# Performance work log

Measured on AMD Instinct MI355X. Metric: run time of the kernel, lower is better.

## Reference

```python
import jax, jax.numpy as jnp
import numpy as np

N_NODES = 50000
N_EDGES = 600000
N_FEAT = 128
HIDDEN = 128
OUT_CH = 128
N_GRAPHS = 64
BN_EPS = 1e-5


def gcn_conv(x, src, dst, ew, W, b):
    """PyG GCNConv: add self-loops, symmetric deg^{-1/2} normalization with edge weights."""
    n = x.shape[0]
    h = x @ W  # [N, out]
    loop = jnp.arange(n)
    src2 = jnp.concatenate([src, loop])
    dst2 = jnp.concatenate([dst, loop])
    w2 = jnp.concatenate([ew, jnp.ones((n,), x.dtype)])
    deg = jax.ops.segment_sum(w2, dst2, num_segments=n)
    dinv = jnp.where(deg > 0, jax.lax.rsqrt(deg), 0.0)
    norm = dinv[src2] * w2 * dinv[dst2]  # [E+N]
    out = jax.ops.segment_sum(h[src2] * norm[:, None], dst2, num_segments=n)
    return out + b


def setup_inputs() -> dict:
    key = jax.random.key(0)
    ks = jax.random.split(key, 12)
    x = jax.random.normal(ks[0], (N_NODES, N_FEAT), jnp.float32)
    edge_index = jax.random.randint(ks[1], (2, N_EDGES), 0, N_NODES, dtype=jnp.int64)
    batch = jnp.sort(jax.random.randint(ks[2], (N_NODES,), 0, N_GRAPHS, dtype=jnp.int64))
    edge_attr = jax.random.uniform(ks[3], (N_EDGES,), jnp.float32)
    s1 = 1.0 / np.sqrt(N_FEAT)
    s2 = 1.0 / np.sqrt(HIDDEN)
    s3 = 1.0 / np.sqrt(OUT_CH)
    s4 = 1.0 / np.sqrt(OUT_CH // 2)
    return {
        "x": x, "edge_index": edge_index, "batch": batch, "edge_attr": edge_attr,
        "W1": jax.random.uniform(ks[4], (N_FEAT, HIDDEN), jnp.float32, -s1, s1),
        "b1": jnp.zeros((HIDDEN,), jnp.float32),
        "W2": jax.random.uniform(ks[5], (HIDDEN, OUT_CH), jnp.float32, -s2, s2),
        "b2": jnp.zeros((OUT_CH,), jnp.float32),
        "fc1_W": jax.random.uniform(ks[6], (OUT_CH, OUT_CH // 2), jnp.float32, -s3, s3),
        "fc1_b": jax.random.uniform(ks[7], (OUT_CH // 2,), jnp.float32, -s3, s3),
        "bn_gamma": jnp.ones((OUT_CH // 2,), jnp.float32),
        "bn_beta": jnp.zeros((OUT_CH // 2,), jnp.float32),
        "fc3_W": jax.random.uniform(ks[8], (OUT_CH // 2, 1), jnp.float32, -s4, s4),
        "fc3_b": jax.random.uniform(ks[9], (1,), jnp.float32, -s4, s4),
    }


def reference(x, edge_index, batch, edge_attr, W1, b1, W2, b2,
              fc1_W, fc1_b, bn_gamma, bn_beta, fc3_W, fc3_b):
    src, dst = edge_index[0], edge_index[1]
    h = jax.nn.relu(gcn_conv(x, src, dst, edge_attr, W1, b1))
    # dropout skipped (deterministic eval: mode=False)
    h = jax.nn.relu(gcn_conv(h, src, dst, edge_attr, W2, b2))
    # global_mean_pool over batch segment ids
    sums = jax.ops.segment_sum(h, batch, num_segments=N_GRAPHS)  # [G, out]
    cnt = jax.ops.segment_sum(jnp.ones_like(batch, jnp.float32), batch, num_segments=N_GRAPHS)
    g = sums / jnp.maximum(cnt, 1.0)[:, None]
    z = jax.nn.relu(g @ fc1_W + fc1_b)
    # BatchNorm1d with batch statistics (training-mode math, biased var)
    mean = jnp.mean(z, axis=0)
    var = jnp.mean((z - mean) ** 2, axis=0)
    z = bn_gamma * (z - mean) * jax.lax.rsqrt(var + BN_EPS) + bn_beta
    return z @ fc3_W + fc3_b  # [G, 1]
```

## Files before the change

kernel.cpp:

```cpp
#include <hip/hip_runtime.h>

#define NNODES 50000
#define NEDGES 600000
#define NGRAPHS 64
#define BN_EPS 1e-5f
#define NB1 ((NNODES + 255) / 256)
#define PPG 16
#define GEMM_BLOCKS ((NNODES + 127) / 128)
#define COUNT_BLOCKS 512


__device__ __forceinline__ void gemm_tile(const float* __restrict__ A,
        const float* __restrict__ W, float* __restrict__ C, int block) {
    __shared__ float a_lds[32][132];
    __shared__ float w_lds[32][192];
    const int tid = threadIdx.x;
    const int row0 = block * 128;
    const int tx = tid & 15;
    const int ty = tid >> 4;
    float acc[8][8];
#pragma unroll
    for (int i = 0; i < 8; ++i)
#pragma unroll
        for (int j = 0; j < 8; ++j) acc[i][j] = 0.f;

    for (int kc = 0; kc < 128; kc += 32) {
#pragma unroll
        for (int p = 0; p < 4; ++p) {
            int idx = p * 256 + tid;
            int r = idx >> 3;
            int k4 = (idx & 7) << 2;
            int grow = row0 + r;
            float4 v = make_float4(0.f, 0.f, 0.f, 0.f);
            if (grow < NNODES) v = *(const float4*)(A + (size_t)grow * 128 + kc + k4);
            a_lds[k4 + 0][r] = v.x; a_lds[k4 + 1][r] = v.y;
            a_lds[k4 + 2][r] = v.z; a_lds[k4 + 3][r] = v.w;
        }
#pragma unroll
        for (int p = 0; p < 4; ++p) {
            int idx = p * 256 + tid;
            int kk = idx >> 5;
            int c4 = idx & 31;
            float4 v = *(const float4*)(W + (size_t)(kc + kk) * 128 + c4 * 4);
            int sw = 12 * (c4 >> 1) + ((c4 & 1) << 2);
            *(float4*)&w_lds[kk][sw] = v;
        }
        __syncthreads();
#pragma unroll
        for (int k = 0; k < 32; ++k) {
            float a[8], b[8];
            *(float4*)&a[0] = *(const float4*)&a_lds[k][ty * 8];
            *(float4*)&a[4] = *(const float4*)&a_lds[k][ty * 8 + 4];
            *(float4*)&b[0] = *(const float4*)&w_lds[k][tx * 12];
            *(float4*)&b[4] = *(const float4*)&w_lds[k][tx * 12 + 4];
#pragma unroll
            for (int i = 0; i < 8; ++i)
#pragma unroll
                for (int j = 0; j < 8; ++j)
                    acc[i][j] = fmaf(a[i], b[j], acc[i][j]);
        }
        __syncthreads();
    }
#pragma unroll
    for (int i = 0; i < 8; ++i) {
        int grow = row0 + ty * 8 + i;
        if (grow < NNODES) {
            float4 v0 = make_float4(acc[i][0], acc[i][1], acc[i][2], acc[i][3]);
            float4 v1 = make_float4(acc[i][4], acc[i][5], acc[i][6], acc[i][7]);
            *(float4*)(C + (size_t)grow * 128 + tx * 8) = v0;
            *(float4*)(C + (size_t)grow * 128 + tx * 8 + 4) = v1;
        }
    }
}

__global__ __launch_bounds__(256) void k_gemm1_count(const float* __restrict__ A,
        const float* __restrict__ W, float* __restrict__ C,
        const int* __restrict__ dst, int* __restrict__ cnt, int* __restrict__ rank) {
    if (blockIdx.x >= GEMM_BLOCKS) {
        int b = blockIdx.x - GEMM_BLOCKS;
        for (int e = b * 256 + threadIdx.x; e < NEDGES; e += COUNT_BLOCKS * 256) {
            int d = dst[e];
            rank[e] = atomicAdd(&cnt[d], 1);
        }
        return;
    }
    gemm_tile(A, W, C, blockIdx.x);
}

__global__ __launch_bounds__(256) void k_gemm(const float* __restrict__ A,
        const float* __restrict__ W, float* __restrict__ C) {
    gemm_tile(A, W, C, blockIdx.x);
}


__global__ __launch_bounds__(256) void k_scan1(const int* __restrict__ cnt,
        int* __restrict__ excl, int* __restrict__ bsum) {
    __shared__ int sh[256];
    int b = blockIdx.x, t = threadIdx.x;
    int idx = b * 256 + t;
    int v = (idx < NNODES) ? cnt[idx] : 0;
    sh[t] = v;
    __syncthreads();
#pragma unroll
    for (int off = 1; off < 256; off <<= 1) {
        int x = (t >= off) ? sh[t - off] : 0;
        __syncthreads();
        sh[t] += x;
        __syncthreads();
    }
    if (idx < NNODES) excl[idx] = sh[t] - v;
    if (t == 255) bsum[b] = sh[255];
}

__global__ __launch_bounds__(256) void k_scan2(int* __restrict__ bsum) {
    __shared__ int sh[256];
    int t = threadIdx.x;
    int v = (t < NB1) ? bsum[t] : 0;
    sh[t] = v;
    __syncthreads();
#pragma unroll
    for (int off = 1; off < 256; off <<= 1) {
        int x = (t >= off) ? sh[t - off] : 0;
        __syncthreads();
        sh[t] += x;
        __syncthreads();
    }
    if (t < NB1) bsum[t] = sh[t] - v;
}

__global__ __launch_bounds__(256) void k_scan3(const int* __restrict__ excl,
        const int* __restrict__ bsum, int* __restrict__ row_start) {
    int b = blockIdx.x, t = threadIdx.x;
    int idx = b * 256 + t;
    if (idx < NNODES) row_start[idx] = excl[idx] + bsum[b];
    if (idx == 0) row_start[NNODES] = NEDGES;
}


__global__ __launch_bounds__(256) void k_place(const int* __restrict__ src,
        const int* __restrict__ dst, const float* __restrict__ ew,
        const int* __restrict__ rank, const int* __restrict__ row_start,
        int2* __restrict__ csr_pk) {
    int e = blockIdx.x * 256 + threadIdx.x;
    if (e < NEDGES) {
        int d = dst[e];
        int slot = row_start[d] + rank[e];
        csr_pk[slot] = make_int2(src[e], __float_as_int(ew[e]));
    }
}

__global__ __launch_bounds__(256) void k_deg(const int* __restrict__ row_start,
        const int2* __restrict__ csr_pk, float* __restrict__ dinv) {
    int i = blockIdx.x * 256 + threadIdx.x;
    if (i >= NNODES) return;
    int e0 = row_start[i], e1 = row_start[i + 1];
    float deg = 1.f;
    for (int e = e0; e < e1; ++e) deg += __int_as_float(csr_pk[e].y);
    dinv[i] = rsqrtf(deg);
}

__global__ __launch_bounds__(256) void k_wfill(const int* __restrict__ row_start,
        int2* __restrict__ csr_pk, const float* __restrict__ dinv) {
    int i = blockIdx.x * 256 + threadIdx.x;
    if (i >= NNODES) return;
    int e0 = row_start[i], e1 = row_start[i + 1];
    float di = dinv[i];
    for (int e = e0; e < e1; ++e) {
        int2 pk = csr_pk[e];
        float w = dinv[pk.x] * __int_as_float(pk.y) * di;
        csr_pk[e].y = __float_as_int(w);
    }
}


__global__ __launch_bounds__(256) void k_aggregate(const float* __restrict__ h,
        const float* __restrict__ dinv, const int* __restrict__ row_start,
        const int2* __restrict__ csr_pk, const float* __restrict__ bias,
        float* __restrict__ out) {
    int gtid = blockIdx.x * 256 + threadIdx.x;
    int i = gtid >> 5;
    int lane = (gtid & 31) << 2;
    if (i >= NNODES) return;
    float di = dinv[i];
    float sw = di * di;
    float4 hv = *(const float4*)(h + (size_t)i * 128 + lane);
    float ax = sw * hv.x, ay = sw * hv.y, az = sw * hv.z, aw = sw * hv.w;
    int e = row_start[i];
    int e1 = row_start[i + 1];
    for (; e + 3 < e1; e += 4) {
        int2 p0 = csr_pk[e], p1 = csr_pk[e + 1], p2 = csr_pk[e + 2], p3 = csr_pk[e + 3];
        float4 v0 = *(const float4*)(h + (size_t)p0.x * 128 + lane);
        float4 v1 = *(const float4*)(h + (size_t)p1.x * 128 + lane);
        float4 v2 = *(const float4*)(h + (size_t)p2.x * 128 + lane);
        float4 v3 = *(const float4*)(h + (size_t)p3.x * 128 + lane);
        float w0 = __int_as_float(p0.y), w1 = __int_as_float(p1.y);
        float w2 = __int_as_float(p2.y), w3 = __int_as_float(p3.y);
        ax = fmaf(w0, v0.x, ax); ay = fmaf(w0, v0.y, ay);
        az = fmaf(w0, v0.z, az); aw = fmaf(w0, v0.w, aw);
        ax = fmaf(w1, v1.x, ax); ay = fmaf(w1, v1.y, ay);
        az = fmaf(w1, v1.z, az); aw = fmaf(w1, v1.w, aw);
        ax = fmaf(w2, v2.x, ax); ay = fmaf(w2, v2.y, ay);
        az = fmaf(w2, v2.z, az); aw = fmaf(w2, v2.w, aw);
        ax = fmaf(w3, v3.x, ax); ay = fmaf(w3, v3.y, ay);
        az = fmaf(w3, v3.z, az); aw = fmaf(w3, v3.w, aw);
    }
    for (; e < e1; ++e) {
        int2 p0 = csr_pk[e];
        float w0 = __int_as_float(p0.y);
        float4 v0 = *(const float4*)(h + (size_t)p0.x * 128 + lane);
        ax = fmaf(w0, v0.x, ax); ay = fmaf(w0, v0.y, ay);
        az = fmaf(w0, v0.z, az); aw = fmaf(w0, v0.w, aw);
    }
    float4 b = *(const float4*)(bias + lane);
    float4 o;
    o.x = fmaxf(ax + b.x, 0.f);
    o.y = fmaxf(ay + b.y, 0.f);
    o.z = fmaxf(az + b.z, 0.f);
    o.w = fmaxf(aw + b.w, 0.f);
    *(float4*)(out + (size_t)i * 128 + lane) = o;
}


__global__ __launch_bounds__(256) void k_pool1(const float* __restrict__ h2,
        const int* __restrict__ batch, float* __restrict__ part) {
    __shared__ float sh[256];
    int g = blockIdx.x / PPG;
    int p = blockIdx.x % PPG;
    int t = threadIdx.x;
    int lo = 0, hi = NNODES;
    while (lo < hi) { int mid = (lo + hi) >> 1; if (batch[mid] < g) lo = mid + 1; else hi = mid; }
    int b0 = lo;
    lo = 0; hi = NNODES;
    int g1 = g + 1;
    while (lo < hi) { int mid = (lo + hi) >> 1; if (batch[mid] < g1) lo = mid + 1; else hi = mid; }
    int b1 = lo;

    int c = t & 127, q = t >> 7;
    float acc = 0.f;
    for (int r = b0 + p * 2 + q; r < b1; r += PPG * 2) acc += h2[(size_t)r * 128 + c];
    sh[t] = acc;
    __syncthreads();
    if (t < 128) part[((size_t)g * PPG + p) * 128 + t] = sh[t] + sh[t + 128];
}

__global__ __launch_bounds__(128) void k_pool2(const float* __restrict__ part,
        const int* __restrict__ batch, float* __restrict__ gmean) {
    int g = blockIdx.x;
    int t = threadIdx.x;
    int lo = 0, hi = NNODES;
    while (lo < hi) { int mid = (lo + hi) >> 1; if (batch[mid] < g) lo = mid + 1; else hi = mid; }
    int b0 = lo;
    lo = 0; hi = NNODES;
    int g1 = g + 1;
    while (lo < hi) { int mid = (lo + hi) >> 1; if (batch[mid] < g1) lo = mid + 1; else hi = mid; }
    int b1 = lo;
    float s = 0.f;
#pragma unroll
    for (int p = 0; p < PPG; ++p) s += part[((size_t)g * PPG + p) * 128 + t];
    float n = (float)(b1 - b0);
    gmean[g * 128 + t] = s / fmaxf(n, 1.f);
}


__global__ __launch_bounds__(256) void k_head(const float* __restrict__ gmean,
        const float* __restrict__ fc1W, const float* __restrict__ fc1b,
        const float* __restrict__ gamma, const float* __restrict__ beta,
        const float* __restrict__ fc3W, const float* __restrict__ fc3b,
        float* __restrict__ out) {
    __shared__ float z[64][65];
    __shared__ float mu[64], isd[64];
    int t = threadIdx.x;
    int r = t >> 2;
    int c0 = (t & 3) * 16;
    float acc[16];
#pragma unroll
    for (int j = 0; j < 16; ++j) acc[j] = 0.f;
    for (int k = 0; k < 128; ++k) {
        float gv = gmean[r * 128 + k];
#pragma unroll
        for (int j = 0; j < 16; ++j) acc[j] = fmaf(gv, fc1W[k * 64 + c0 + j], acc[j]);
    }
#pragma unroll
    for (int j = 0; j < 16; ++j)
        z[r][c0 + j] = fmaxf(acc[j] + fc1b[c0 + j], 0.f);
    __syncthreads();
    if (t < 64) {
        float m = 0.f;
        for (int rr = 0; rr < 64; ++rr) m += z[rr][t];
        m *= (1.f / 64.f);
        float v = 0.f;
        for (int rr = 0; rr < 64; ++rr) { float d = z[rr][t] - m; v = fmaf(d, d, v); }
        v *= (1.f / 64.f);
        mu[t] = m;
        isd[t] = rsqrtf(v + BN_EPS);
    }
    __syncthreads();
    if (t < 64) {
        float a2 = fc3b[0];
        for (int cc = 0; cc < 64; ++cc) {
            float zn = fmaf(gamma[cc] * (z[t][cc] - mu[cc]), isd[cc], beta[cc]);
            a2 = fmaf(zn, fc3W[cc], a2);
        }
        out[t] = a2;
    }
}


extern "C" void kernel_launch(void* const* d_in, const int* in_sizes, int n_in,
                              void* d_out, int out_size, void* d_ws, size_t ws_size,
                              hipStream_t stream) {
    const float* x    = (const float*)d_in[0];
    const int*   ei   = (const int*)d_in[1];
    const int*   batch= (const int*)d_in[2];
    const float* ew   = (const float*)d_in[3];
    const float* W1   = (const float*)d_in[4];
    const float* b1   = (const float*)d_in[5];
    const float* W2   = (const float*)d_in[6];
    const float* b2   = (const float*)d_in[7];
    const float* fc1W = (const float*)d_in[8];
    const float* fc1b = (const float*)d_in[9];
    const float* gam  = (const float*)d_in[10];
    const float* bet  = (const float*)d_in[11];
    const float* fc3W = (const float*)d_in[12];
    const float* fc3b = (const float*)d_in[13];
    float* out = (float*)d_out;
    const int* srcp = ei;
    const int* dstp = ei + NEDGES;

    char* wsb = (char*)d_ws;
    size_t off = 0;
    auto alloc = [&](size_t bytes) {
        void* p = wsb + off;
        off = (off + bytes + 255) & ~(size_t)255;
        return p;
    };
    float* dinv      = (float*)alloc(NNODES * 4);
    int*   row_start = (int*)alloc((NNODES + 1) * 4);
    int*   cnt       = (int*)alloc(NNODES * 4);
    int*   excl      = (int*)alloc(NNODES * 4);
    int*   bsum      = (int*)alloc(NB1 * 4);
    int*   rank      = (int*)alloc((size_t)NEDGES * 4);
    int2*  csr_pk    = (int2*)alloc((size_t)NEDGES * 8);
    float* hbuf      = (float*)alloc((size_t)NNODES * 128 * 4);
    float* abuf      = (float*)alloc((size_t)NNODES * 128 * 4);
    float* part      = (float*)alloc((size_t)NGRAPHS * PPG * 128 * 4);
    float* gmean     = (float*)alloc(NGRAPHS * 128 * 4);
    (void)ws_size; (void)in_sizes; (void)n_in; (void)out_size;

    const int nb_edges = (NEDGES + 255) / 256;

    hipMemsetAsync(cnt, 0, NNODES * 4, stream);
    k_gemm1_count<<<GEMM_BLOCKS + COUNT_BLOCKS, 256, 0, stream>>>(x, W1, hbuf, dstp, cnt, rank);
    k_scan1<<<NB1, 256, 0, stream>>>(cnt, excl, bsum);
    k_scan2<<<1, 256, 0, stream>>>(bsum);
    k_scan3<<<NB1, 256, 0, stream>>>(excl, bsum, row_start);
    k_place<<<nb_edges, 256, 0, stream>>>(srcp, dstp, ew, rank, row_start, csr_pk);
    k_deg<<<NB1, 256, 0, stream>>>(row_start, csr_pk, dinv);
    k_wfill<<<NB1, 256, 0, stream>>>(row_start, csr_pk, dinv);

    k_aggregate<<<(NNODES * 32 + 255) / 256, 256, 0, stream>>>(hbuf, dinv, row_start,
                                                               csr_pk, b1, abuf);
    k_gemm<<<GEMM_BLOCKS, 256, 0, stream>>>(abuf, W2, hbuf);
    k_aggregate<<<(NNODES * 32 + 255) / 256, 256, 0, stream>>>(hbuf, dinv, row_start,
                                                               csr_pk, b2, abuf);
    k_pool1<<<NGRAPHS * PPG, 256, 0, stream>>>(abuf, batch, part);
    k_pool2<<<NGRAPHS, 128, 0, stream>>>(part, batch, gmean);
    k_head<<<1, 256, 0, stream>>>(gmean, fc1W, fc1b, gam, bet, fc3W, fc3b, out);
}
```

Before: 267.5 us.

## Build CSR via range-owned LDS histograms, retile GEMM to 512 threads, fuse pool2 into head

Edge-to-CSR construction now uses 64 blocks that each own a range of destination nodes. Each block scans all edges, counts with LDS atomics and then places edge ids through an order array, replacing global atomics, the rank array and the memset. The GEMM tile moves to 512 threads with 4x8 accumulators per thread, and the pool2 reduction is folded into the head kernel. The cost is that each owner block reads the full dst array, and the CSR fill is now a separate gather pass.

```diff
diff --git a/kernel.cpp b/kernel.cpp
--- a/kernel.cpp
+++ b/kernel.cpp
@@ -7,7 +7,8 @@
 #define NB1 ((NNODES + 255) / 256)
 #define PPG 16
 #define GEMM_BLOCKS ((NNODES + 127) / 128)
-#define COUNT_BLOCKS 512
+#define NOWN 64
+#define RANGE 782
 
 
 __device__ __forceinline__ void gemm_tile(const float* __restrict__ A,
@@ -18,16 +19,16 @@
     const int row0 = block * 128;
     const int tx = tid & 15;
     const int ty = tid >> 4;
-    float acc[8][8];
-#pragma unroll
-    for (int i = 0; i < 8; ++i)
+    float acc[4][8];
+#pragma unroll
+    for (int i = 0; i < 4; ++i)
 #pragma unroll
         for (int j = 0; j < 8; ++j) acc[i][j] = 0.f;
 
     for (int kc = 0; kc < 128; kc += 32) {
 #pragma unroll
-        for (int p = 0; p < 4; ++p) {
-            int idx = p * 256 + tid;
+        for (int p = 0; p < 2; ++p) {
+            int idx = p * 512 + tid;
             int r = idx >> 3;
             int k4 = (idx & 7) << 2;
             int grow = row0 + r;
@@ -37,8 +38,8 @@
             a_lds[k4 + 2][r] = v.z; a_lds[k4 + 3][r] = v.w;
         }
 #pragma unroll
-        for (int p = 0; p < 4; ++p) {
-            int idx = p * 256 + tid;
+        for (int p = 0; p < 2; ++p) {
+            int idx = p * 512 + tid;
             int kk = idx >> 5;
             int c4 = idx & 31;
             float4 v = *(const float4*)(W + (size_t)(kc + kk) * 128 + c4 * 4);
@@ -48,13 +49,12 @@
         __syncthreads();
 #pragma unroll
         for (int k = 0; k < 32; ++k) {
-            float a[8], b[8];
-            *(float4*)&a[0] = *(const float4*)&a_lds[k][ty * 8];
-            *(float4*)&a[4] = *(const float4*)&a_lds[k][ty * 8 + 4];
+            float a[4], b[8];
+            *(float4*)&a[0] = *(const float4*)&a_lds[k][ty * 4];
             *(float4*)&b[0] = *(const float4*)&w_lds[k][tx * 12];
             *(float4*)&b[4] = *(const float4*)&w_lds[k][tx * 12 + 4];
 #pragma unroll
-            for (int i = 0; i < 8; ++i)
+            for (int i = 0; i < 4; ++i)
 #pragma unroll
                 for (int j = 0; j < 8; ++j)
                     acc[i][j] = fmaf(a[i], b[j], acc[i][j]);
@@ -62,8 +62,8 @@
         __syncthreads();
     }
 #pragma unroll
-    for (int i = 0; i < 8; ++i) {
-        int grow = row0 + ty * 8 + i;
+    for (int i = 0; i < 4; ++i) {
+        int grow = row0 + ty * 4 + i;
         if (grow < NNODES) {
             float4 v0 = make_float4(acc[i][0], acc[i][1], acc[i][2], acc[i][3]);
             float4 v1 = make_float4(acc[i][4], acc[i][5], acc[i][6], acc[i][7]);
@@ -73,21 +73,36 @@
     }
 }
 
-__global__ __launch_bounds__(256) void k_gemm1_count(const float* __restrict__ A,
+__global__ __launch_bounds__(512) void k_gemm1_hist(const float* __restrict__ A,
         const float* __restrict__ W, float* __restrict__ C,
-        const int* __restrict__ dst, int* __restrict__ cnt, int* __restrict__ rank) {
-    if (blockIdx.x >= GEMM_BLOCKS) {
-        int b = blockIdx.x - GEMM_BLOCKS;
-        for (int e = b * 256 + threadIdx.x; e < NEDGES; e += COUNT_BLOCKS * 256) {
-            int d = dst[e];
-            rank[e] = atomicAdd(&cnt[d], 1);
-        }
+        const int* __restrict__ dst, int* __restrict__ cnt_g) {
+    if (blockIdx.x < NOWN) {
+        __shared__ int lh[RANGE];
+        int t = threadIdx.x;
+        int lo = blockIdx.x * RANGE;
+        int n = min(RANGE, NNODES - lo);
+        for (int i = t; i < RANGE; i += 512) lh[i] = 0;
+        __syncthreads();
+        const int4* d4 = (const int4*)dst;
+        for (int q = t; q < NEDGES / 4; q += 512) {
+            int4 v = d4[q];
+            unsigned a0 = (unsigned)(v.x - lo);
+            unsigned a1 = (unsigned)(v.y - lo);
+            unsigned a2 = (unsigned)(v.z - lo);
+            unsigned a3 = (unsigned)(v.w - lo);
+            if (a0 < (unsigned)n) atomicAdd(&lh[a0], 1);
+            if (a1 < (unsigned)n) atomicAdd(&lh[a1], 1);
+            if (a2 < (unsigned)n) atomicAdd(&lh[a2], 1);
+            if (a3 < (unsigned)n) atomicAdd(&lh[a3], 1);
+        }
+        __syncthreads();
+        for (int i = t; i < n; i += 512) cnt_g[lo + i] = lh[i];
         return;
     }
-    gemm_tile(A, W, C, blockIdx.x);
-}
-
-__global__ __launch_bounds__(256) void k_gemm(const float* __restrict__ A,
+    gemm_tile(A, W, C, blockIdx.x - NOWN);
+}
+
+__global__ __launch_bounds__(512) void k_gemm(const float* __restrict__ A,
         const float* __restrict__ W, float* __restrict__ C) {
     gemm_tile(A, W, C, blockIdx.x);
 }
@@ -137,15 +152,36 @@
 }
 
 
-__global__ __launch_bounds__(256) void k_place(const int* __restrict__ src,
-        const int* __restrict__ dst, const float* __restrict__ ew,
-        const int* __restrict__ rank, const int* __restrict__ row_start,
+__global__ __launch_bounds__(512) void k_place_own(const int* __restrict__ dst,
+        const int* __restrict__ row_start, int* __restrict__ order) {
+    __shared__ int lh[RANGE];
+    int t = threadIdx.x;
+    int lo = blockIdx.x * RANGE;
+    int n = min(RANGE, NNODES - lo);
+    for (int i = t; i < RANGE; i += 512) lh[i] = 0;
+    __syncthreads();
+    const int4* d4 = (const int4*)dst;
+    for (int q = t; q < NEDGES / 4; q += 512) {
+        int4 v = d4[q];
+        int e = q * 4;
+        unsigned a0 = (unsigned)(v.x - lo);
+        unsigned a1 = (unsigned)(v.y - lo);
+        unsigned a2 = (unsigned)(v.z - lo);
+        unsigned a3 = (unsigned)(v.w - lo);
+        if (a0 < (unsigned)n) { int tk = atomicAdd(&lh[a0], 1); order[row_start[v.x] + tk] = e; }
+        if (a1 < (unsigned)n) { int tk = atomicAdd(&lh[a1], 1); order[row_start[v.y] + tk] = e + 1; }
+        if (a2 < (unsigned)n) { int tk = atomicAdd(&lh[a2], 1); order[row_start[v.z] + tk] = e + 2; }
+        if (a3 < (unsigned)n) { int tk = atomicAdd(&lh[a3], 1); order[row_start[v.w] + tk] = e + 3; }
+    }
+}
+
+__global__ __launch_bounds__(256) void k_fill(const int* __restrict__ order,
+        const int* __restrict__ src, const float* __restrict__ ew,
         int2* __restrict__ csr_pk) {
-    int e = blockIdx.x * 256 + threadIdx.x;
-    if (e < NEDGES) {
-        int d = dst[e];
-        int slot = row_start[d] + rank[e];
-        csr_pk[slot] = make_int2(src[e], __float_as_int(ew[e]));
+    int s = blockIdx.x * 256 + threadIdx.x;
+    if (s < NEDGES) {
+        int e = order[s];
+        csr_pk[s] = make_int2(src[e], __float_as_int(ew[e]));
     }
 }
 
@@ -243,40 +279,43 @@
     if (t < 128) part[((size_t)g * PPG + p) * 128 + t] = sh[t] + sh[t + 128];
 }
 
-__global__ __launch_bounds__(128) void k_pool2(const float* __restrict__ part,
-        const int* __restrict__ batch, float* __restrict__ gmean) {
-    int g = blockIdx.x;
-    int t = threadIdx.x;
-    int lo = 0, hi = NNODES;
-    while (lo < hi) { int mid = (lo + hi) >> 1; if (batch[mid] < g) lo = mid + 1; else hi = mid; }
-    int b0 = lo;
-    lo = 0; hi = NNODES;
-    int g1 = g + 1;
-    while (lo < hi) { int mid = (lo + hi) >> 1; if (batch[mid] < g1) lo = mid + 1; else hi = mid; }
-    int b1 = lo;
-    float s = 0.f;
-#pragma unroll
-    for (int p = 0; p < PPG; ++p) s += part[((size_t)g * PPG + p) * 128 + t];
-    float n = (float)(b1 - b0);
-    gmean[g * 128 + t] = s / fmaxf(n, 1.f);
-}
-
-
-__global__ __launch_bounds__(256) void k_head(const float* __restrict__ gmean,
+
+__global__ __launch_bounds__(256) void k_head(const float* __restrict__ part,
+        const int* __restrict__ batch,
         const float* __restrict__ fc1W, const float* __restrict__ fc1b,
         const float* __restrict__ gamma, const float* __restrict__ beta,
         const float* __restrict__ fc3W, const float* __restrict__ fc3b,
         float* __restrict__ out) {
+    __shared__ float g[64][129];
     __shared__ float z[64][65];
     __shared__ float mu[64], isd[64];
+    __shared__ float cntg[64];
     int t = threadIdx.x;
+    if (t < 64) {
+        int lo = 0, hi = NNODES;
+        while (lo < hi) { int mid = (lo + hi) >> 1; if (batch[mid] < t) lo = mid + 1; else hi = mid; }
+        int b0 = lo;
+        lo = 0; hi = NNODES;
+        int g1 = t + 1;
+        while (lo < hi) { int mid = (lo + hi) >> 1; if (batch[mid] < g1) lo = mid + 1; else hi = mid; }
+        cntg[t] = fmaxf((float)(lo - b0), 1.f);
+    }
+    __syncthreads();
+    for (int idx = t; idx < 64 * 128; idx += 256) {
+        int gg = idx >> 7, c = idx & 127;
+        float s = 0.f;
+#pragma unroll
+        for (int p = 0; p < PPG; ++p) s += part[((size_t)gg * PPG + p) * 128 + c];
+        g[gg][c] = s / cntg[gg];
+    }
+    __syncthreads();
     int r = t >> 2;
     int c0 = (t & 3) * 16;
     float acc[16];
 #pragma unroll
     for (int j = 0; j < 16; ++j) acc[j] = 0.f;
     for (int k = 0; k < 128; ++k) {
-        float gv = gmean[r * 128 + k];
+        float gv = g[r][k];
 #pragma unroll
         for (int j = 0; j < 16; ++j) acc[j] = fmaf(gv, fc1W[k * 64 + c0 + j], acc[j]);
     }
@@ -336,34 +375,30 @@
     };
     float* dinv      = (float*)alloc(NNODES * 4);
     int*   row_start = (int*)alloc((NNODES + 1) * 4);
-    int*   cnt       = (int*)alloc(NNODES * 4);
+    int*   cnt_g     = (int*)alloc(NNODES * 4);
     int*   excl      = (int*)alloc(NNODES * 4);
     int*   bsum      = (int*)alloc(NB1 * 4);
-    int*   rank      = (int*)alloc((size_t)NEDGES * 4);
+    int*   order     = (int*)alloc((size_t)NEDGES * 4);
     int2*  csr_pk    = (int2*)alloc((size_t)NEDGES * 8);
     float* hbuf      = (float*)alloc((size_t)NNODES * 128 * 4);
     float* abuf      = (float*)alloc((size_t)NNODES * 128 * 4);
     float* part      = (float*)alloc((size_t)NGRAPHS * PPG * 128 * 4);
-    float* gmean     = (float*)alloc(NGRAPHS * 128 * 4);
     (void)ws_size; (void)in_sizes; (void)n_in; (void)out_size;
 
-    const int nb_edges = (NEDGES + 255) / 256;
-
-    hipMemsetAsync(cnt, 0, NNODES * 4, stream);
-    k_gemm1_count<<<GEMM_BLOCKS + COUNT_BLOCKS, 256, 0, stream>>>(x, W1, hbuf, dstp, cnt, rank);
-    k_scan1<<<NB1, 256, 0, stream>>>(cnt, excl, bsum);
+    k_gemm1_hist<<<NOWN + GEMM_BLOCKS, 512, 0, stream>>>(x, W1, hbuf, dstp, cnt_g);
+    k_scan1<<<NB1, 256, 0, stream>>>(cnt_g, excl, bsum);
     k_scan2<<<1, 256, 0, stream>>>(bsum);
     k_scan3<<<NB1, 256, 0, stream>>>(excl, bsum, row_start);
-    k_place<<<nb_edges, 256, 0, stream>>>(srcp, dstp, ew, rank, row_start, csr_pk);
+    k_place_own<<<NOWN, 512, 0, stream>>>(dstp, row_start, order);
+    k_fill<<<(NEDGES + 255) / 256, 256, 0, stream>>>(order, srcp, ew, csr_pk);
     k_deg<<<NB1, 256, 0, stream>>>(row_start, csr_pk, dinv);
     k_wfill<<<NB1, 256, 0, stream>>>(row_start, csr_pk, dinv);
 
     k_aggregate<<<(NNODES * 32 + 255) / 256, 256, 0, stream>>>(hbuf, dinv, row_start,
                                                                csr_pk, b1, abuf);
-    k_gemm<<<GEMM_BLOCKS, 256, 0, stream>>>(abuf, W2, hbuf);
+    k_gemm<<<GEMM_BLOCKS, 512, 0, stream>>>(abuf, W2, hbuf);
     k_aggregate<<<(NNODES * 32 + 255) / 256, 256, 0, stream>>>(hbuf, dinv, row_start,
                                                                csr_pk, b2, abuf);
     k_pool1<<<NGRAPHS * PPG, 256, 0, stream>>>(abuf, batch, part);
-    k_pool2<<<NGRAPHS, 128, 0, stream>>>(part, batch, gmean);
-    k_head<<<1, 256, 0, stream>>>(gmean, fc1W, fc1b, gam, bet, fc3W, fc3b, out);
-}
+    k_head<<<1, 256, 0, stream>>>(part, batch, fc1W, fc1b, gam, bet, fc3W, fc3b, out);
+}
```

Result: slower. 520.0 us (+94.4%).
